# Kernel optimization log

Hardware: AMD Instinct MI355X
Metric: run time of the kernel (lower is better)

The kernel has to match this reference:

```python
import jax, jax.numpy as jnp
import numpy as np

WS = 7      # window_size
NH = 8      # num_heads
ND = 5      # n_degree -> Np = 6


def setup_inputs() -> dict:
    key = jax.random.key(0)
    ks = jax.random.split(key, 9)
    B, Q, C, H, W = 2, 100, 256, 64, 64
    Np = ND + 1
    ws2 = WS * WS
    return {
        "x": jax.random.normal(ks[0], (B, C, H, W), dtype=jnp.float32),
        "polys": jax.random.uniform(ks[1], (B, Q, 2, Np), dtype=jnp.float32),
        "w_qkv": jax.random.normal(ks[2], (3 * C, C), dtype=jnp.float32) * 0.02,
        "b_qkv": jnp.zeros((3 * C,), dtype=jnp.float32),
        "w_proj": jax.random.normal(ks[3], (C, C), dtype=jnp.float32) * 0.02,
        "b_proj": jnp.zeros((C,), dtype=jnp.float32),
        "conv_w": jax.random.normal(ks[4], (1, ws2, 1, 1), dtype=jnp.float32) * 0.1,
        "conv_b": jnp.zeros((1,), dtype=jnp.float32),
        "pos_bias": jax.random.normal(ks[5], (ws2, 1), dtype=jnp.float32),
    }


def reference(x, polys, w_qkv, b_qkv, w_proj, b_proj, conv_w, conv_b, pos_bias):
    B, C, H, W = x.shape
    _, Q, _, Np = polys.shape  # polys: [B,Q,2,n_degree+1]
    ws = WS
    ws2 = ws * ws
    nh = NH
    hd = C // nh
    scale = hd ** -0.5

    # --- polynomial -> sample points (get_points) ---
    alpha = jnp.linspace(0.0, 1.0, Np)
    alphas = jnp.stack([alpha ** i for i in range(Np - 1, -1, -1)], axis=1)  # [Np, Np]
    points = jnp.swapaxes(polys @ alphas.T, -1, -2)  # [B,Q,Np,2]
    points = 2.0 * points - 1.0
    points = points[:, :, None, :, :]  # [B,Q,1,Np,2]

    # --- deformable window grid (faithful to torch, incl. -ws//2 floor-div) ---
    lo = (-ws) // 2   # -4 for ws=7
    hi = ws // 2      #  3
    delta_h = 2.0 * jnp.linspace(lo, hi, ws) / H
    delta_w = 2.0 * jnp.linspace(lo, hi, ws) / W
    mesh_x, mesh_y = jnp.meshgrid(delta_w, delta_h, indexing='xy')  # [ws,ws]
    mesh_x = mesh_x.reshape(-1, 1)  # [ws2,1]
    mesh_y = mesh_y.reshape(-1, 1)
    grid_y = points[..., 0] + mesh_y  # [B,Q,ws2,Np]
    grid_x = points[..., 1] + mesh_x
    grid = jnp.stack((grid_y, grid_x), axis=-1)        # [B,Q,ws2,Np,2]
    grid = grid.reshape(B, Q * Np * ws2, 2)            # same flat order as torch .view

    # --- grid_sample: bilinear, zeros padding, align_corners=True ---
    # grid[...,0] -> x coordinate (width), grid[...,1] -> y (height)
    def sample_one(img, g):  # img [C,H,W], g [P,2] -> [C,P]
        fx = (g[:, 0] + 1.0) * 0.5 * (W - 1)
        fy = (g[:, 1] + 1.0) * 0.5 * (H - 1)
        x0 = jnp.floor(fx)
        y0 = jnp.floor(fy)
        wx1 = fx - x0
        wy1 = fy - y0

        def gather(yy, xx):
            valid = (xx >= 0) & (xx <= W - 1) & (yy >= 0) & (yy <= H - 1)
            xi = jnp.clip(xx, 0, W - 1).astype(jnp.int32)
            yi = jnp.clip(yy, 0, H - 1).astype(jnp.int32)
            return img[:, yi, xi] * valid.astype(img.dtype)  # [C,P]

        v00 = gather(y0, x0)
        v01 = gather(y0, x0 + 1)
        v10 = gather(y0 + 1, x0)
        v11 = gather(y0 + 1, x0 + 1)
        return (v00 * (1 - wy1) * (1 - wx1) + v01 * (1 - wy1) * wx1 +
                v10 * wy1 * (1 - wx1) + v11 * wy1 * wx1)

    sampled = jax.vmap(sample_one)(x, grid)            # [B, C, Q*Np*ws2]
    sampled = sampled.reshape(B, C, Q * Np, ws2)
    sampled = jnp.transpose(sampled, (0, 2, 1, 3))     # [B, Q*Np, C, ws2]
    sp = sampled.reshape(B, Q, Np, C, ws2)
    sp = jnp.transpose(sp, (0, 1, 2, 4, 3)).reshape(B, Q * Np, ws2, C)

    # --- windowed multi-head self-attention over each sampled patch ---
    qkv = sp @ w_qkv.T + b_qkv                          # [B,QN,ws2,3C]
    qkv = qkv.reshape(B, Q * Np, ws2, 3, nh, hd)
    qkv = jnp.transpose(qkv, (3, 0, 4, 1, 2, 5))        # [3,B,nh,QN,ws2,hd]
    q, k, v = qkv[0], qkv[1], qkv[2]
    attn = jnp.einsum('bhnpd,bhnqd->bhnpq', q, k) * scale
    attn = attn + pos_bias.reshape(1, 1, 1, ws2, 1)     # bias per query row (as in torch)
    attn = jax.nn.softmax(attn, axis=-1)
    o = jnp.einsum('bhnpq,bhnqd->bhnpd', attn, v)       # [B,nh,QN,ws2,hd]
    o = jnp.swapaxes(o, 2, 3)                           # [B,nh,ws2,QN,hd]
    o = o.reshape(B, Q * Np, ws2, C)                    # faithful torch .reshape
    o = jnp.swapaxes(o, 1, 2)                           # [B,ws2,QN,C]

    # --- conv1x1 over the ws2 channel axis, then output projection ---
    y = jnp.einsum('bwnc,w->bnc', o, conv_w.reshape(ws2)) + conv_b.reshape(1, 1, 1)
    y = y @ w_proj.T + b_proj                           # [B,QN,C]
    return y.reshape(B, Q, Np, C)
```

## Files before the change

### kernel.cpp

```cpp
#include <hip/hip_runtime.h>

#define B_    2
#define QN    100
#define NP    6
#define WS2   49
#define CC    256
#define NHH   8
#define HDD   32
#define NWIN  600

#define XT_BYTES   (8388608 + 1024)
#define ZABS       2097152
#define WB_BYTES   393216
#define WPT_BYTES  262144

#define SPB_LD 264

#define QK_LD  72
#define VT_LD  72
#define P_LD   72
#define OW_LD  36
#define QK_SHORTS   (WS2 * QK_LD)
#define WREG_SHORTS (QK_SHORTS + 32 * VT_LD)

typedef __attribute__((ext_vector_type(8))) short bf16x8;
typedef __attribute__((ext_vector_type(4))) float f32x4;

__device__ __forceinline__ unsigned short f2bf(float f) {
  union { float f; unsigned int i; } v; v.f = f;
  unsigned int x = v.i;
  x += 0x7fffu + ((x >> 16) & 1u);
  return (unsigned short)(x >> 16);
}
__device__ __forceinline__ float bf2f(unsigned short u) {
  union { unsigned int i; float f; } v; v.i = ((unsigned int)u) << 16; return v.f;
}

__global__ void k0_prep(const float* __restrict__ x, float* __restrict__ xT,
                        const float* __restrict__ w_qkv, unsigned short* __restrict__ wbp,
                        const float* __restrict__ w_proj, float* __restrict__ wpT) {
  __shared__ float tile[32][33];
  const int gb = blockIdx.x;
  if (gb < 2048) {
    int b   = gb >> 10;
    int rem = gb & 1023;
    int hw0 = (rem & 127) * 32;
    int c0  = (rem >> 7) * 32;
    int tx = threadIdx.x & 31, ty = threadIdx.x >> 5;
    const float* src = x + (size_t)b * CC * 4096;
    float* dst = xT + (size_t)b * 4096 * CC;
    #pragma unroll
    for (int i = ty; i < 32; i += 8)
      tile[i][tx] = src[(size_t)(c0 + i) * 4096 + hw0 + tx];
    __syncthreads();
    #pragma unroll
    for (int i = ty; i < 32; i += 8)
      dst[(size_t)(hw0 + i) * CC + c0 + tx] = tile[tx][i];
  } else if (gb < 2144) {
    int g = (gb - 2048) * 256 + threadIdx.x;
    int lane = g & 63;
    int ks = (g >> 6) & 7;
    int nt = g >> 9;
    int n  = nt * 16 + (lane & 15);
    int k0 = ks * 32 + (lane >> 4) * 8;
    const float* src = w_qkv + (size_t)n * CC + k0;
    float4 lo = *(const float4*)(src);
    float4 hi = *(const float4*)(src + 4);
    unsigned short o[8] = { f2bf(lo.x), f2bf(lo.y), f2bf(lo.z), f2bf(lo.w),
                            f2bf(hi.x), f2bf(hi.y), f2bf(hi.z), f2bf(hi.w) };
    *(uint4*)(wbp + (size_t)g * 8) = *(uint4*)o;
  } else if (gb == 2144) {
    xT[ZABS + threadIdx.x] = 0.0f;
  } else {
    int t = gb - 2145;
    int r0 = (t >> 3) * 32;
    int c0 = (t & 7) * 32;
    int tx = threadIdx.x & 31, ty = threadIdx.x >> 5;
    #pragma unroll
    for (int i = ty; i < 32; i += 8)
      tile[i][tx] = w_proj[(size_t)(r0 + i) * CC + c0 + tx];
    __syncthreads();
    #pragma unroll
    for (int i = ty; i < 32; i += 8)
      wpT[(size_t)(c0 + i) * CC + r0 + tx] = tile[tx][i];
  }
}

__device__ __forceinline__ void attn_head(
    const bf16x8 qf[4], const bf16x8 kf[4],
    unsigned short* P, const unsigned short* Vt, float* Ow, unsigned short* ob16,
    int lane, int lm, int lg) {
  const float scale = 0.17677669529663687f;
  f32x4 s[4][4];
  #pragma unroll
  for (int mt = 0; mt < 4; mt++)
    #pragma unroll
    for (int nt = 0; nt < 4; nt++) {
      s[mt][nt] = (f32x4){0.f, 0.f, 0.f, 0.f};
      s[mt][nt] = __builtin_amdgcn_mfma_f32_16x16x32_bf16(qf[mt], kf[nt], s[mt][nt], 0, 0, 0);
    }
  #pragma unroll
  for (int mt = 0; mt < 4; mt++)
    #pragma unroll
    for (int nt = 0; nt < 4; nt++) {
      bool badcol = (nt == 3) && (lm > 0);
      #pragma unroll
      for (int reg = 0; reg < 4; reg++)
        s[mt][nt][reg] = badcol ? -1e30f : s[mt][nt][reg] * scale;
    }
  #pragma unroll
  for (int mt = 0; mt < 4; mt++) {
    #pragma unroll
    for (int reg = 0; reg < 4; reg++) {
      float mx = fmaxf(fmaxf(s[mt][0][reg], s[mt][1][reg]),
                       fmaxf(s[mt][2][reg], s[mt][3][reg]));
      #pragma unroll
      for (int off = 1; off < 16; off <<= 1) mx = fmaxf(mx, __shfl_xor(mx, off));
      float sum = 0.0f;
      #pragma unroll
      for (int nt = 0; nt < 4; nt++) {
        float e = __expf(s[mt][nt][reg] - mx);
        s[mt][nt][reg] = e;
        sum += e;
      }
      #pragma unroll
      for (int off = 1; off < 16; off <<= 1) sum += __shfl_xor(sum, off);
      float inv = 1.0f / sum;
      #pragma unroll
      for (int nt = 0; nt < 4; nt++) s[mt][nt][reg] *= inv;
    }
  }
  #pragma unroll
  for (int mt = 0; mt < 4; mt++)
    #pragma unroll
    for (int nt = 0; nt < 4; nt++)
      #pragma unroll
      for (int reg = 0; reg < 4; reg++) {
        int p = mt * 16 + lg * 4 + reg;
        if (p < WS2) P[p * P_LD + nt * 16 + lm] = f2bf(s[mt][nt][reg]);
      }
  f32x4 o[4][2];
  #pragma unroll
  for (int mt = 0; mt < 4; mt++)
    #pragma unroll
    for (int nt2 = 0; nt2 < 2; nt2++) o[mt][nt2] = (f32x4){0.f, 0.f, 0.f, 0.f};
  #pragma unroll
  for (int ks = 0; ks < 2; ks++) {
    bf16x8 vf[2];
    #pragma unroll
    for (int nt2 = 0; nt2 < 2; nt2++)
      vf[nt2] = *(const bf16x8*)(Vt + (nt2 * 16 + lm) * VT_LD + ks * 32 + lg * 8);
    #pragma unroll
    for (int mt = 0; mt < 4; mt++) {
      bf16x8 af = *(const bf16x8*)(P + (mt * 16 + lm) * P_LD + ks * 32 + lg * 8);
      #pragma unroll
      for (int nt2 = 0; nt2 < 2; nt2++)
        o[mt][nt2] = __builtin_amdgcn_mfma_f32_16x16x32_bf16(af, vf[nt2], o[mt][nt2], 0, 0, 0);
    }
  }
  #pragma unroll
  for (int mt = 0; mt < 4; mt++)
    #pragma unroll
    for (int reg = 0; reg < 4; reg++) {
      int p = mt * 16 + lg * 4 + reg;
      if (p < WS2) {
        #pragma unroll
        for (int nt2 = 0; nt2 < 2; nt2++)
          Ow[p * OW_LD + nt2 * 16 + lm] = o[mt][nt2][reg];
      }
    }
  for (int idx = lane; idx < WS2 * 4; idx += 64) {
    int p = idx >> 2, seg = idx & 3;
    const float* src = Ow + p * OW_LD + seg * 8;
    unsigned short o8[8];
    #pragma unroll
    for (int k = 0; k < 8; k++) o8[k] = f2bf(src[k]);
    *(uint4*)(ob16 + (size_t)idx * 8) = *(uint4*)o8;
  }
}

__launch_bounds__(256, 2)
__global__ void k12_fused(const float* __restrict__ xT,
                          const float* __restrict__ polys,
                          const unsigned short* __restrict__ wbp,
                          const float* __restrict__ b_qkv,
                          unsigned short* __restrict__ o16) {
  __shared__ __align__(16) unsigned short spb[64 * SPB_LD];
  __shared__ __align__(16) unsigned short wreg[4][WREG_SHORTS];
  int*   co_off = (int*)&wreg[0][0];
  float* co_w   = (float*)&wreg[0][0] + 196;
  const int tid = threadIdx.x;
  const int m = blockIdx.x;
  const int b = blockIdx.y;
  const int lane = tid & 63;
  const int wv = tid >> 6;
  const int lm = lane & 15;
  const int lg = lane >> 4;
  unsigned short* myq = &wreg[wv][0];
  unsigned short* VtW = myq + QK_SHORTS;

  if (tid < WS2) {
    int n = m * WS2 + tid;
    int q = n / (WS2 * NP);
    int p = (n / NP) % WS2;
    int a = n % NP;
    const float* pc = polys + (size_t)(b * QN + q) * 12;
    float al = (float)a * 0.2f;
    float py = pc[0];
    float px = pc[6];
    #pragma unroll
    for (int i = 1; i < 6; i++) { py = py * al + pc[i]; px = px * al + pc[6 + i]; }
    py = 2.0f * py - 1.0f;
    px = 2.0f * px - 1.0f;
    float gy = py + (2.0f * (-4.0f + (float)(p / 7) * (7.0f / 6.0f))) * (1.0f / 64.0f);
    float gx = px + (2.0f * (-4.0f + (float)(p % 7) * (7.0f / 6.0f))) * (1.0f / 64.0f);
    float fx = (gy + 1.0f) * 0.5f * 63.0f;
    float fy = (gx + 1.0f) * 0.5f * 63.0f;
    float x0 = floorf(fx), y0 = floorf(fy);
    float wx = fx - x0, wy = fy - y0;
    float x1 = x0 + 1.0f, y1 = y0 + 1.0f;
    int xi0 = (int)fminf(fmaxf(x0, 0.0f), 63.0f);
    int yi0 = (int)fminf(fmaxf(y0, 0.0f), 63.0f);
    int xi1 = (int)fminf(fmaxf(x1, 0.0f), 63.0f);
    int yi1 = (int)fminf(fmaxf(y1, 0.0f), 63.0f);
    bool vx0 = (x0 >= 0.0f) && (x0 <= 63.0f);
    bool vx1 = (x1 >= 0.0f) && (x1 <= 63.0f);
    bool vy0 = (y0 >= 0.0f) && (y0 <= 63.0f);
    bool vy1 = (y1 >= 0.0f) && (y1 <= 63.0f);
    const int bb = b * 4096;
    co_off[tid * 4 + 0] = (vx0 && vy0) ? (bb + yi0 * 64 + xi0) * CC : ZABS;
    co_off[tid * 4 + 1] = (vx1 && vy0) ? (bb + yi0 * 64 + xi1) * CC : ZABS;
    co_off[tid * 4 + 2] = (vx0 && vy1) ? (bb + yi1 * 64 + xi0) * CC : ZABS;
    co_off[tid * 4 + 3] = (vx1 && vy1) ? (bb + yi1 * 64 + xi1) * CC : ZABS;
    co_w[tid * 4 + 0] = (1.0f - wy) * (1.0f - wx);
    co_w[tid * 4 + 1] = (1.0f - wy) * wx;
    co_w[tid * 4 + 2] = wy * (1.0f - wx);
    co_w[tid * 4 + 3] = wy * wx;
  }
  {
    unsigned int* z = (unsigned int*)(spb + WS2 * SPB_LD);
    for (int i = tid; i < 15 * SPB_LD / 2; i += 256) z[i] = 0u;
  }
  {
    unsigned int* vz = (unsigned int*)VtW;
    #pragma unroll
    for (int i = 0; i < 18; i++) vz[i * 64 + lane] = 0u;
  }
  __syncthreads();

  for (int bi = 0; bi < 6; bi++) {
    const int rbase = bi * 8;
    float vv[8][4];
    #pragma unroll
    for (int k = 0; k < 8; k++) {
      int r = rbase + k;
      int4 off = *(const int4*)&co_off[r * 4];
      vv[k][0] = xT[off.x + tid];
      vv[k][1] = xT[off.y + tid];
      vv[k][2] = xT[off.z + tid];
      vv[k][3] = xT[off.w + tid];
    }
    #pragma unroll
    for (int k = 0; k < 8; k++) {
      int r = rbase + k;
      float4 w = *(const float4*)&co_w[r * 4];
      float s = vv[k][0] * w.x + vv[k][1] * w.y + vv[k][2] * w.z + vv[k][3] * w.w;
      spb[r * SPB_LD + tid] = f2bf(s);
    }
  }
  {
    int4 off = *(const int4*)&co_off[48 * 4];
    float4 w = *(const float4*)&co_w[48 * 4];
    float s = xT[off.x + tid] * w.x + xT[off.y + tid] * w.y
            + xT[off.z + tid] * w.z + xT[off.w + tid] * w.w;
    spb[48 * SPB_LD + tid] = f2bf(s);
  }
  __syncthreads();

  unsigned short* obase = o16 + (size_t)(b * NWIN + m) * 392 * 32;

  for (int hp = 0; hp < 2; hp++) {
    const int h = 2 * wv + hp;
    for (int jc = 0; jc < 3; jc++) {
      const int nt0 = jc * 16 + 2 * h;
      f32x4 acc[4][2];
      #pragma unroll
      for (int j4 = 0; j4 < 2; j4++) {
        float bias = b_qkv[(nt0 + j4) * 16 + lm];
        #pragma unroll
        for (int mt = 0; mt < 4; mt++) acc[mt][j4] = (f32x4){bias, bias, bias, bias};
      }
      bf16x8 bnx[2];
      #pragma unroll
      for (int j4 = 0; j4 < 2; j4++)
        bnx[j4] = *(const bf16x8*)(wbp + (size_t)(((nt0 + j4) * 8 + 0) * 64 + lane) * 8);
      #pragma unroll
      for (int ks = 0; ks < 8; ks++) {
        bf16x8 bc[2];
        #pragma unroll
        for (int j4 = 0; j4 < 2; j4++) bc[j4] = bnx[j4];
        if (ks < 7) {
          #pragma unroll
          for (int j4 = 0; j4 < 2; j4++)
            bnx[j4] = *(const bf16x8*)(wbp + (size_t)(((nt0 + j4) * 8 + ks + 1) * 64 + lane) * 8);
        }
        bf16x8 af[4];
        #pragma unroll
        for (int mt = 0; mt < 4; mt++)
          af[mt] = *(const bf16x8*)(spb + (mt * 16 + lm) * SPB_LD + ks * 32 + lg * 8);
        #pragma unroll
        for (int j4 = 0; j4 < 2; j4++)
          #pragma unroll
          for (int mt = 0; mt < 4; mt++)
            acc[mt][j4] = __builtin_amdgcn_mfma_f32_16x16x32_bf16(af[mt], bc[j4], acc[mt][j4], 0, 0, 0);
      }
      if (jc < 2) {
        const int cb = jc * 32;
        #pragma unroll
        for (int mt = 0; mt < 4; mt++)
          #pragma unroll
          for (int reg = 0; reg < 4; reg++) {
            int rr = mt * 16 + lg * 4 + reg;
            if (rr < WS2) {
              #pragma unroll
              for (int j4 = 0; j4 < 2; j4++)
                myq[rr * QK_LD + cb + j4 * 16 + lm] = f2bf(acc[mt][j4][reg]);
            }
          }
      } else {
        #pragma unroll
        for (int mt = 0; mt < 4; mt++)
          #pragma unroll
          for (int reg = 0; reg < 4; reg++) {
            int rr = mt * 16 + lg * 4 + reg;
            if (rr < WS2) {
              #pragma unroll
              for (int j4 = 0; j4 < 2; j4++)
                VtW[(j4 * 16 + lm) * VT_LD + rr] = f2bf(acc[mt][j4][reg]);
            }
          }
      }
    }

    bf16x8 qf[4], kf[4];
    #pragma unroll
    for (int t = 0; t < 4; t++) {
      int r = t * 16 + lm; if (r > 48) r = 48;
      const unsigned short* row = myq + r * QK_LD;
      qf[t] = *(const bf16x8*)(row + lg * 8);
      kf[t] = *(const bf16x8*)(row + 32 + lg * 8);
    }
    unsigned short* P = myq;
    float* Ow = (float*)myq;
    attn_head(qf, kf, P, VtW, Ow,
              obase + (size_t)h * WS2 * HDD, lane, lm, lg);
  }
}

__global__ void k3_conv_proj(const unsigned short* __restrict__ o16,
                             const float* __restrict__ conv_w,
                             const float* __restrict__ conv_b,
                             const float* __restrict__ wpT,
                             const float* __restrict__ b_proj,
                             float* __restrict__ out) {
  __shared__ float yv[CC];
  __shared__ float cw[WS2];
  __shared__ int atab[392];
  const int tid = threadIdx.x;
  const int np = blockIdx.x;
  const int b = blockIdx.y;
  if (tid < WS2) cw[tid] = conv_w[tid];
  for (int i = tid; i < 392; i += 256) {
    int Q = np * 392 + i;
    int m = Q % 600;
    int hp = Q / 600;
    atab[i] = ((b * NWIN + m) * 392 + hp) * 32;
  }
  __syncthreads();
  const int cg = tid >> 5, dd = tid & 31;
  float acc = conv_b[0];
  for (int p = 0; p < WS2; p++)
    acc += cw[p] * bf2f(o16[(size_t)atab[p * 8 + cg] + dd]);
  yv[tid] = acc;
  __syncthreads();
  const float* wp = wpT + tid;
  float a0 = 0.0f, a1 = 0.0f, a2 = 0.0f, a3 = 0.0f;
  #pragma unroll 8
  for (int c = 0; c < CC; c += 4) {
    float4 y4 = *(const float4*)&yv[c];
    a0 += y4.x * wp[(c + 0) * CC];
    a1 += y4.y * wp[(c + 1) * CC];
    a2 += y4.z * wp[(c + 2) * CC];
    a3 += y4.w * wp[(c + 3) * CC];
  }
  out[((size_t)(b * NWIN + np)) * CC + tid] = b_proj[tid] + ((a0 + a1) + (a2 + a3));
}

extern "C" void kernel_launch(void* const* d_in, const int* in_sizes, int n_in,
                              void* d_out, int out_size, void* d_ws, size_t ws_size,
                              hipStream_t stream) {
  const float* x        = (const float*)d_in[0];
  const float* polys    = (const float*)d_in[1];
  const float* w_qkv    = (const float*)d_in[2];
  const float* b_qkv    = (const float*)d_in[3];
  const float* w_proj   = (const float*)d_in[4];
  const float* b_proj   = (const float*)d_in[5];
  const float* conv_w   = (const float*)d_in[6];
  const float* conv_b   = (const float*)d_in[7];
  float* out = (float*)d_out;

  char* ws = (char*)d_ws;
  float* xT = (float*)ws;
  unsigned short* wbp = (unsigned short*)(ws + XT_BYTES);
  float* wpT = (float*)(ws + XT_BYTES + WB_BYTES);
  unsigned short* o16 = (unsigned short*)(ws + XT_BYTES + WB_BYTES + WPT_BYTES);

  hipLaunchKernelGGL(k0_prep, dim3(2209), dim3(256), 0, stream, x, xT, w_qkv, wbp, w_proj, wpT);
  hipLaunchKernelGGL(k12_fused, dim3(NWIN, B_), dim3(256), 0, stream,
                     xT, polys, wbp, b_qkv, o16);
  hipLaunchKernelGGL(k3_conv_proj, dim3(NWIN, B_), dim3(256), 0, stream,
                     o16, conv_w, conv_b, wpT, b_proj, out);
}
```

Baseline: 176.5 us.

## Keep V in registers via shuffles, swizzle LDS, reorder output layout for conv

```diff
diff --git a/kernel.cpp b/kernel.cpp
--- a/kernel.cpp
+++ b/kernel.cpp
@@ -16,12 +16,7 @@
 
 #define SPB_LD 264
 
-#define QK_LD  72
-#define VT_LD  72
-#define P_LD   72
-#define OW_LD  36
-#define QK_SHORTS   (WS2 * QK_LD)
-#define WREG_SHORTS (QK_SHORTS + 32 * VT_LD)
+#define RG_SHORTS (WS2 * 64)
 
 typedef __attribute__((ext_vector_type(8))) short bf16x8;
 typedef __attribute__((ext_vector_type(4))) float f32x4;
@@ -34,6 +29,9 @@
 }
 __device__ __forceinline__ float bf2f(unsigned short u) {
   union { unsigned int i; float f; } v; v.i = ((unsigned int)u) << 16; return v.f;
+}
+__device__ __forceinline__ unsigned int pk2(float a, float b) {
+  return (unsigned int)f2bf(a) | ((unsigned int)f2bf(b) << 16);
 }
 
 __global__ void k0_prep(const float* __restrict__ x, float* __restrict__ xT,
@@ -86,121 +84,27 @@
   }
 }
 
-__device__ __forceinline__ void attn_head(
-    const bf16x8 qf[4], const bf16x8 kf[4],
-    unsigned short* P, const unsigned short* Vt, float* Ow, unsigned short* ob16,
-    int lane, int lm, int lg) {
-  const float scale = 0.17677669529663687f;
-  f32x4 s[4][4];
-  #pragma unroll
-  for (int mt = 0; mt < 4; mt++)
-    #pragma unroll
-    for (int nt = 0; nt < 4; nt++) {
-      s[mt][nt] = (f32x4){0.f, 0.f, 0.f, 0.f};
-      s[mt][nt] = __builtin_amdgcn_mfma_f32_16x16x32_bf16(qf[mt], kf[nt], s[mt][nt], 0, 0, 0);
-    }
-  #pragma unroll
-  for (int mt = 0; mt < 4; mt++)
-    #pragma unroll
-    for (int nt = 0; nt < 4; nt++) {
-      bool badcol = (nt == 3) && (lm > 0);
-      #pragma unroll
-      for (int reg = 0; reg < 4; reg++)
-        s[mt][nt][reg] = badcol ? -1e30f : s[mt][nt][reg] * scale;
-    }
-  #pragma unroll
-  for (int mt = 0; mt < 4; mt++) {
-    #pragma unroll
-    for (int reg = 0; reg < 4; reg++) {
-      float mx = fmaxf(fmaxf(s[mt][0][reg], s[mt][1][reg]),
-                       fmaxf(s[mt][2][reg], s[mt][3][reg]));
-      #pragma unroll
-      for (int off = 1; off < 16; off <<= 1) mx = fmaxf(mx, __shfl_xor(mx, off));
-      float sum = 0.0f;
-      #pragma unroll
-      for (int nt = 0; nt < 4; nt++) {
-        float e = __expf(s[mt][nt][reg] - mx);
-        s[mt][nt][reg] = e;
-        sum += e;
-      }
-      #pragma unroll
-      for (int off = 1; off < 16; off <<= 1) sum += __shfl_xor(sum, off);
-      float inv = 1.0f / sum;
-      #pragma unroll
-      for (int nt = 0; nt < 4; nt++) s[mt][nt][reg] *= inv;
-    }
-  }
-  #pragma unroll
-  for (int mt = 0; mt < 4; mt++)
-    #pragma unroll
-    for (int nt = 0; nt < 4; nt++)
-      #pragma unroll
-      for (int reg = 0; reg < 4; reg++) {
-        int p = mt * 16 + lg * 4 + reg;
-        if (p < WS2) P[p * P_LD + nt * 16 + lm] = f2bf(s[mt][nt][reg]);
-      }
-  f32x4 o[4][2];
-  #pragma unroll
-  for (int mt = 0; mt < 4; mt++)
-    #pragma unroll
-    for (int nt2 = 0; nt2 < 2; nt2++) o[mt][nt2] = (f32x4){0.f, 0.f, 0.f, 0.f};
-  #pragma unroll
-  for (int ks = 0; ks < 2; ks++) {
-    bf16x8 vf[2];
-    #pragma unroll
-    for (int nt2 = 0; nt2 < 2; nt2++)
-      vf[nt2] = *(const bf16x8*)(Vt + (nt2 * 16 + lm) * VT_LD + ks * 32 + lg * 8);
-    #pragma unroll
-    for (int mt = 0; mt < 4; mt++) {
-      bf16x8 af = *(const bf16x8*)(P + (mt * 16 + lm) * P_LD + ks * 32 + lg * 8);
-      #pragma unroll
-      for (int nt2 = 0; nt2 < 2; nt2++)
-        o[mt][nt2] = __builtin_amdgcn_mfma_f32_16x16x32_bf16(af, vf[nt2], o[mt][nt2], 0, 0, 0);
-    }
-  }
-  #pragma unroll
-  for (int mt = 0; mt < 4; mt++)
-    #pragma unroll
-    for (int reg = 0; reg < 4; reg++) {
-      int p = mt * 16 + lg * 4 + reg;
-      if (p < WS2) {
-        #pragma unroll
-        for (int nt2 = 0; nt2 < 2; nt2++)
-          Ow[p * OW_LD + nt2 * 16 + lm] = o[mt][nt2][reg];
-      }
-    }
-  for (int idx = lane; idx < WS2 * 4; idx += 64) {
-    int p = idx >> 2, seg = idx & 3;
-    const float* src = Ow + p * OW_LD + seg * 8;
-    unsigned short o8[8];
-    #pragma unroll
-    for (int k = 0; k < 8; k++) o8[k] = f2bf(src[k]);
-    *(uint4*)(ob16 + (size_t)idx * 8) = *(uint4*)o8;
-  }
-}
-
-__launch_bounds__(256, 2)
+__launch_bounds__(256, 3)
 __global__ void k12_fused(const float* __restrict__ xT,
                           const float* __restrict__ polys,
                           const unsigned short* __restrict__ wbp,
                           const float* __restrict__ b_qkv,
                           unsigned short* __restrict__ o16) {
-  __shared__ __align__(16) unsigned short spb[64 * SPB_LD];
-  __shared__ __align__(16) unsigned short wreg[4][WREG_SHORTS];
-  int*   co_off = (int*)&wreg[0][0];
-  float* co_w   = (float*)&wreg[0][0] + 196;
+  __shared__ __align__(16) unsigned short spb[WS2 * SPB_LD];
+  __shared__ __align__(16) unsigned short wreg[4 * RG_SHORTS];
+  int*   co_off = (int*)wreg;
+  float* co_w   = (float*)wreg + 196;
   const int tid = threadIdx.x;
-  const int m = blockIdx.x;
+  const int mm = (blockIdx.x & 7) * 75 + (blockIdx.x >> 3);
   const int b = blockIdx.y;
   const int lane = tid & 63;
   const int wv = tid >> 6;
   const int lm = lane & 15;
   const int lg = lane >> 4;
-  unsigned short* myq = &wreg[wv][0];
-  unsigned short* VtW = myq + QK_SHORTS;
+  unsigned short* myreg = wreg + wv * RG_SHORTS;
 
   if (tid < WS2) {
-    int n = m * WS2 + tid;
+    int n = mm * WS2 + tid;
     int q = n / (WS2 * NP);
     int p = (n / NP) % WS2;
     int a = n % NP;
@@ -237,15 +141,6 @@
     co_w[tid * 4 + 2] = wy * (1.0f - wx);
     co_w[tid * 4 + 3] = wy * wx;
   }
-  {
-    unsigned int* z = (unsigned int*)(spb + WS2 * SPB_LD);
-    for (int i = tid; i < 15 * SPB_LD / 2; i += 256) z[i] = 0u;
-  }
-  {
-    unsigned int* vz = (unsigned int*)VtW;
-    #pragma unroll
-    for (int i = 0; i < 18; i++) vz[i * 64 + lane] = 0u;
-  }
   __syncthreads();
 
   for (int bi = 0; bi < 6; bi++) {
@@ -277,10 +172,20 @@
   }
   __syncthreads();
 
-  unsigned short* obase = o16 + (size_t)(b * NWIN + m) * 392 * 32;
+  int rowb[4];
+  #pragma unroll
+  for (int mt = 0; mt < 4; mt++) {
+    int r = mt * 16 + lm; if (r > 48) r = 48;
+    rowb[mt] = r * SPB_LD;
+  }
+
+  const size_t boff = (size_t)b * 235200;
+  const float scale = 0.17677669529663687f;
 
   for (int hp = 0; hp < 2; hp++) {
     const int h = 2 * wv + hp;
+    unsigned int vpk[4][2][2];
+
     for (int jc = 0; jc < 3; jc++) {
       const int nt0 = jc * 16 + 2 * h;
       f32x4 acc[4][2];
@@ -307,7 +212,7 @@
         bf16x8 af[4];
         #pragma unroll
         for (int mt = 0; mt < 4; mt++)
-          af[mt] = *(const bf16x8*)(spb + (mt * 16 + lm) * SPB_LD + ks * 32 + lg * 8);
+          af[mt] = *(const bf16x8*)(spb + rowb[mt] + ks * 32 + lg * 8);
         #pragma unroll
         for (int j4 = 0; j4 < 2; j4++)
           #pragma unroll
@@ -323,21 +228,19 @@
             int rr = mt * 16 + lg * 4 + reg;
             if (rr < WS2) {
               #pragma unroll
-              for (int j4 = 0; j4 < 2; j4++)
-                myq[rr * QK_LD + cb + j4 * 16 + lm] = f2bf(acc[mt][j4][reg]);
+              for (int j4 = 0; j4 < 2; j4++) {
+                int c = cb + j4 * 16 + lm;
+                myreg[rr * 64 + ((((c >> 3) ^ (rr & 7)) << 3) | (c & 7))] = f2bf(acc[mt][j4][reg]);
+              }
             }
           }
       } else {
         #pragma unroll
         for (int mt = 0; mt < 4; mt++)
           #pragma unroll
-          for (int reg = 0; reg < 4; reg++) {
-            int rr = mt * 16 + lg * 4 + reg;
-            if (rr < WS2) {
-              #pragma unroll
-              for (int j4 = 0; j4 < 2; j4++)
-                VtW[(j4 * 16 + lm) * VT_LD + rr] = f2bf(acc[mt][j4][reg]);
-            }
+          for (int j4 = 0; j4 < 2; j4++) {
+            vpk[mt][j4][0] = pk2(acc[mt][j4][0], acc[mt][j4][1]);
+            vpk[mt][j4][1] = pk2(acc[mt][j4][2], acc[mt][j4][3]);
           }
       }
     }
@@ -346,14 +249,117 @@
     #pragma unroll
     for (int t = 0; t < 4; t++) {
       int r = t * 16 + lm; if (r > 48) r = 48;
-      const unsigned short* row = myq + r * QK_LD;
-      qf[t] = *(const bf16x8*)(row + lg * 8);
-      kf[t] = *(const bf16x8*)(row + 32 + lg * 8);
-    }
-    unsigned short* P = myq;
-    float* Ow = (float*)myq;
-    attn_head(qf, kf, P, VtW, Ow,
-              obase + (size_t)h * WS2 * HDD, lane, lm, lg);
+      const unsigned short* row = myreg + r * 64;
+      qf[t] = *(const bf16x8*)(row + ((lg ^ (r & 7)) << 3));
+      kf[t] = *(const bf16x8*)(row + (((4 + lg) ^ (r & 7)) << 3));
+    }
+
+    f32x4 s[4][4];
+    #pragma unroll
+    for (int mt = 0; mt < 4; mt++)
+      #pragma unroll
+      for (int nt = 0; nt < 4; nt++) {
+        s[mt][nt] = (f32x4){0.f, 0.f, 0.f, 0.f};
+        s[mt][nt] = __builtin_amdgcn_mfma_f32_16x16x32_bf16(qf[mt], kf[nt], s[mt][nt], 0, 0, 0);
+      }
+    #pragma unroll
+    for (int mt = 0; mt < 4; mt++)
+      #pragma unroll
+      for (int nt = 0; nt < 4; nt++) {
+        bool badcol = (nt == 3) && (lm > 0);
+        #pragma unroll
+        for (int reg = 0; reg < 4; reg++)
+          s[mt][nt][reg] = badcol ? -1e30f : s[mt][nt][reg] * scale;
+      }
+    #pragma unroll
+    for (int mt = 0; mt < 4; mt++) {
+      #pragma unroll
+      for (int reg = 0; reg < 4; reg++) {
+        float mx = fmaxf(fmaxf(s[mt][0][reg], s[mt][1][reg]),
+                         fmaxf(s[mt][2][reg], s[mt][3][reg]));
+        #pragma unroll
+        for (int off = 1; off < 16; off <<= 1) mx = fmaxf(mx, __shfl_xor(mx, off));
+        float sum = 0.0f;
+        #pragma unroll
+        for (int nt = 0; nt < 4; nt++) {
+          float e = __expf(s[mt][nt][reg] - mx);
+          s[mt][nt][reg] = e;
+          sum += e;
+        }
+        #pragma unroll
+        for (int off = 1; off < 16; off <<= 1) sum += __shfl_xor(sum, off);
+        float inv = 1.0f / sum;
+        #pragma unroll
+        for (int nt = 0; nt < 4; nt++) s[mt][nt][reg] *= inv;
+      }
+    }
+    #pragma unroll
+    for (int mt = 0; mt < 4; mt++)
+      #pragma unroll
+      for (int nt = 0; nt < 4; nt++)
+        #pragma unroll
+        for (int reg = 0; reg < 4; reg++) {
+          int p = mt * 16 + lg * 4 + reg;
+          if (p < WS2) {
+            int c = nt * 16 + lm;
+            myreg[p * 64 + ((((c >> 3) ^ (p & 7)) << 3) | (c & 7))] = f2bf(s[mt][nt][reg]);
+          }
+        }
+    f32x4 o[4][2];
+    #pragma unroll
+    for (int mt = 0; mt < 4; mt++)
+      #pragma unroll
+      for (int nt2 = 0; nt2 < 2; nt2++) o[mt][nt2] = (f32x4){0.f, 0.f, 0.f, 0.f};
+    const int sA = (lane & 15) + ((lane >> 4) & 1) * 32;
+    const int sB = sA + 16;
+    const int hi = (lane >> 5) & 1;
+    #pragma unroll
+    for (int ks = 0; ks < 2; ks++) {
+      bf16x8 vf[2];
+      #pragma unroll
+      for (int nt2 = 0; nt2 < 2; nt2++) {
+        union { unsigned int u[4]; bf16x8 v; } uu;
+        #pragma unroll
+        for (int w2 = 0; w2 < 2; w2++) {
+          unsigned a0 = __shfl(vpk[2 * ks + 0][nt2][w2], sA);
+          unsigned a1 = __shfl(vpk[2 * ks + 1][nt2][w2], sA);
+          uu.u[w2] = hi ? a1 : a0;
+          unsigned b0 = __shfl(vpk[2 * ks + 0][nt2][w2], sB);
+          unsigned b1 = __shfl(vpk[2 * ks + 1][nt2][w2], sB);
+          uu.u[2 + w2] = hi ? b1 : b0;
+        }
+        vf[nt2] = uu.v;
+      }
+      #pragma unroll
+      for (int mt = 0; mt < 4; mt++) {
+        int r = mt * 16 + lm; if (r > 48) r = 48;
+        bf16x8 af = *(const bf16x8*)(myreg + r * 64 + (((ks * 4 + lg) ^ (r & 7)) << 3));
+        #pragma unroll
+        for (int nt2 = 0; nt2 < 2; nt2++)
+          o[mt][nt2] = __builtin_amdgcn_mfma_f32_16x16x32_bf16(af, vf[nt2], o[mt][nt2], 0, 0, 0);
+      }
+    }
+    float* Ow = (float*)myreg;
+    #pragma unroll
+    for (int mt = 0; mt < 4; mt++)
+      #pragma unroll
+      for (int reg = 0; reg < 4; reg++) {
+        int p = mt * 16 + lg * 4 + reg;
+        if (p < WS2) {
+          #pragma unroll
+          for (int nt2 = 0; nt2 < 2; nt2++)
+            Ow[p * 32 + nt2 * 16 + lm] = o[mt][nt2][reg];
+        }
+      }
+    for (int idx = lane; idx < WS2 * 4; idx += 64) {
+      int p = idx >> 2, seg = idx & 3;
+      const float* src = Ow + p * 32 + seg * 8;
+      unsigned short o8[8];
+      #pragma unroll
+      for (int k = 0; k < 8; k++) o8[k] = f2bf(src[k]);
+      size_t addr = (boff + (size_t)(h * WS2 + p) * 600 + mm) * 32 + seg * 8;
+      *(uint4*)(o16 + addr) = *(uint4*)o8;
+    }
   }
 }
 
@@ -365,22 +371,23 @@
                              float* __restrict__ out) {
   __shared__ float yv[CC];
   __shared__ float cw[WS2];
-  __shared__ int atab[392];
   const int tid = threadIdx.x;
   const int np = blockIdx.x;
   const int b = blockIdx.y;
   if (tid < WS2) cw[tid] = conv_w[tid];
-  for (int i = tid; i < 392; i += 256) {
-    int Q = np * 392 + i;
-    int m = Q % 600;
-    int hp = Q / 600;
-    atab[i] = ((b * NWIN + m) * 392 + hp) * 32;
-  }
   __syncthreads();
-  const int cg = tid >> 5, dd = tid & 31;
+  const unsigned short* wbuf = o16 + ((size_t)b * 235200 + (size_t)np * 392) * 32;
   float acc = conv_b[0];
-  for (int p = 0; p < WS2; p++)
-    acc += cw[p] * bf2f(o16[(size_t)atab[p * 8 + cg] + dd]);
+  #pragma unroll 1
+  for (int pb = 0; pb < 48; pb += 8) {
+    float vals[8];
+    #pragma unroll
+    for (int k = 0; k < 8; k++)
+      vals[k] = bf2f(wbuf[(pb + k) * 256 + tid]);
+    #pragma unroll
+    for (int k = 0; k < 8; k++) acc += cw[pb + k] * vals[k];
+  }
+  acc += cw[48] * bf2f(wbuf[48 * 256 + tid]);
   yv[tid] = acc;
   __syncthreads();
   const float* wp = wpT + tid;
```

Result: slower. 335.1 us (+89.9%).
